# Performance work log

Measured on AMD Instinct MI355X. Metric: run time of the kernel, lower is better.

Reference implementation:

```python
import jax, jax.numpy as jnp
import numpy as np

B, L, D = 16384, 50, 32  # batch, history length, embedding_dim
NU, NI, NC = 100000, 100000, 1000


def setup_inputs() -> dict:
    key = jax.random.key(0)
    ks = jax.random.split(key, 16)
    customer_id = jax.random.randint(ks[0], (B,), 0, NU)
    candidate_good = jax.random.randint(ks[1], (B,), 0, NI)
    candidate_class = jax.random.randint(ks[2], (B,), 0, NC)
    history_goods = jax.random.randint(ks[3], (B, L), 0, NI)
    history_classes = jax.random.randint(ks[4], (B, L), 0, NC)
    user_table = jax.random.normal(ks[5], (NU, D), jnp.float32) * 0.05
    item_table = jax.random.normal(ks[6], (NI, D), jnp.float32) * 0.05
    item_table = item_table.at[0].set(0.0)  # padding_idx=0
    cat_table = jax.random.normal(ks[7], (NC, D), jnp.float32) * 0.05
    cat_table = cat_table.at[0].set(0.0)  # padding_idx=0
    # attention net: Linear(4*2D=256 -> 80), Linear(80 -> 1)
    aw1 = jax.random.normal(ks[8], (4 * 2 * D, 80), jnp.float32) * 0.05
    ab1 = jnp.zeros((80,), jnp.float32)
    aw2 = jax.random.normal(ks[9], (80, 1), jnp.float32) * 0.05
    ab2 = jnp.zeros((1,), jnp.float32)
    # final mlp: 5D=160 -> 256 -> 128 -> 1
    mw1 = jax.random.normal(ks[10], (5 * D, 256), jnp.float32) * 0.05
    mb1 = jnp.zeros((256,), jnp.float32)
    mw2 = jax.random.normal(ks[11], (256, 128), jnp.float32) * 0.05
    mb2 = jnp.zeros((128,), jnp.float32)
    mw3 = jax.random.normal(ks[12], (128, 1), jnp.float32) * 0.05
    mb3 = jnp.zeros((1,), jnp.float32)
    return dict(customer_id=customer_id, candidate_good=candidate_good,
                candidate_class=candidate_class, history_goods=history_goods,
                history_classes=history_classes, user_table=user_table,
                item_table=item_table, cat_table=cat_table,
                aw1=aw1, ab1=ab1, aw2=aw2, ab2=ab2,
                mw1=mw1, mb1=mb1, mw2=mw2, mb2=mb2, mw3=mw3, mb3=mb3)


def reference(customer_id, candidate_good, candidate_class, history_goods,
              history_classes, user_table, item_table, cat_table,
              aw1, ab1, aw2, ab2, mw1, mb1, mw2, mb2, mw3, mb3):
    user_emb = user_table[customer_id]                               # [B, D]
    cand = jnp.concatenate([item_table[candidate_good],
                            cat_table[candidate_class]], axis=-1)    # [B, 2D]
    hist = jnp.concatenate([item_table[history_goods],
                            cat_table[history_classes]], axis=-1)    # [B, L, 2D]
    q = jnp.broadcast_to(cand[:, None, :], hist.shape)               # [B, L, 2D]
    info = jnp.concatenate([q, hist, q - hist, q * hist], axis=-1)   # [B, L, 8D]
    h = jax.nn.relu(info @ aw1 + ab1)                                # [B, L, 80]
    scores = (h @ aw2 + ab2)[..., 0]                                 # [B, L]
    mask = history_goods != 0
    scores = jnp.where(mask, scores, -1e9)
    weights = jax.nn.softmax(scores, axis=1)                         # [B, L]
    att = jnp.einsum('bl,bld->bd', weights, hist)                    # [B, 2D]
    combined = jnp.concatenate([user_emb, cand, att], axis=-1)       # [B, 5D]
    z = jax.nn.relu(combined @ mw1 + mb1)
    z = jax.nn.relu(z @ mw2 + mb2)
    out = (z @ mw3 + mb3)[..., 0]                                    # [B]
    return out
```

## Files before the change

kernel.cpp:

```cpp
#include <hip/hip_runtime.h>
#include <math.h>

#define LHIST 50

typedef __attribute__((ext_vector_type(8))) short bf16x8;
typedef __attribute__((ext_vector_type(4))) float f32x4;

__device__ __forceinline__ unsigned short f2bf(float f) {
    union { float f; unsigned u; } v; v.f = f;
    unsigned r = v.u + 0x7fff + ((v.u >> 16) & 1);
    return (unsigned short)(r >> 16);
}
__device__ __forceinline__ float bf2f(unsigned short h) {
    union { unsigned u; float f; } v; v.u = ((unsigned)h) << 16;
    return v.f;
}


__global__ void prep_kernel(const float* __restrict__ aw1,
                            const float* __restrict__ mw1,
                            const float* __restrict__ mw2,
                            const float* __restrict__ item_table,
                            const float* __restrict__ cat_table,
                            int itemN, int catN,
                            float* __restrict__ Awt,
                            unsigned short* __restrict__ Bmfb,
                            unsigned short* __restrict__ W4fb,
                            unsigned short* __restrict__ W1f,
                            unsigned short* __restrict__ W2f,
                            unsigned short* __restrict__ itemb,
                            unsigned short* __restrict__ catb) {
    int i = blockIdx.x * 256 + threadIdx.x;
    int i8 = i * 8;
    if (i8 + 7 < itemN) {
        float4 a = *(const float4*)&item_table[i8];
        float4 b = *(const float4*)&item_table[i8 + 4];
        ushort4 lo, hi;
        lo.x = f2bf(a.x); lo.y = f2bf(a.y); lo.z = f2bf(a.z); lo.w = f2bf(a.w);
        hi.x = f2bf(b.x); hi.y = f2bf(b.y); hi.z = f2bf(b.z); hi.w = f2bf(b.w);
        *(ushort4*)&itemb[i8] = lo;
        *(ushort4*)&itemb[i8 + 4] = hi;
    }
    if (i8 + 7 < catN) {
        float4 a = *(const float4*)&cat_table[i8];
        float4 b = *(const float4*)&cat_table[i8 + 4];
        ushort4 lo, hi;
        lo.x = f2bf(a.x); lo.y = f2bf(a.y); lo.z = f2bf(a.z); lo.w = f2bf(a.w);
        hi.x = f2bf(b.x); hi.y = f2bf(b.y); hi.z = f2bf(b.z); hi.w = f2bf(b.w);
        *(ushort4*)&catb[i8] = lo;
        *(ushort4*)&catb[i8 + 4] = hi;
    }
    if (i < 5120) {
        int j = i >> 6, k = i & 63;
        Awt[i] = aw1[k * 80 + j] + aw1[(128 + k) * 80 + j];
        int kk = i / 80, n = i - kk * 80;
        int nt = n >> 4, colw = n & 15, ks = kk >> 5, r = kk & 31, qd = r >> 3, off = r & 7;
        int d = ((nt * 2 + ks) * 64 + qd * 16 + colw) * 8 + off;
        Bmfb[d] = f2bf(aw1[(64 + kk) * 80 + n] - aw1[(128 + kk) * 80 + n]);
        W4fb[d] = f2bf(aw1[(192 + kk) * 80 + n]);
    }
    if (i < 40960) {
        int kk = i >> 8, n = i & 255;
        int nt = n >> 4, colw = n & 15, ks = kk >> 5, r = kk & 31, qd = r >> 3, off = r & 7;
        W1f[((nt * 5 + ks) * 64 + qd * 16 + colw) * 8 + off] = f2bf(mw1[i]);
    }
    if (i < 32768) {
        int kk = i >> 7, n = i & 127;
        int nt = n >> 4, colw = n & 15, ks = kk >> 5, r = kk & 31, qd = r >> 3, off = r & 7;
        W2f[((nt * 8 + ks) * 64 + qd * 16 + colw) * 8 + off] = f2bf(mw2[i]);
    }
}

__global__ void __launch_bounds__(256, 6) attn_kernel(
    const int* __restrict__ cid, const int* __restrict__ cg,
    const int* __restrict__ cc,  const int* __restrict__ hg,
    const int* __restrict__ hc,
    const float* __restrict__ user_table, const float* __restrict__ item_table,
    const float* __restrict__ cat_table,
    const float* __restrict__ ab1, const float* __restrict__ aw2,
    const float* __restrict__ Awt, const unsigned short* __restrict__ Bmfb,
    const unsigned short* __restrict__ W4fb,
    const unsigned short* __restrict__ itemb, const unsigned short* __restrict__ catb,
    float* __restrict__ combined)
{
    __shared__ __align__(16) unsigned short sh_Bq[2][5120];
    __shared__ __align__(16) float sh_q[2][64];
    __shared__ float sh_bias[2][80];
    __shared__ float sh_sc[2][64];
    __shared__ float sh_aw2[80];
    __shared__ __align__(16) float sh_att[2][2][64];

    const int t = threadIdx.x;
    const int b0 = blockIdx.x * 2;
    const int wv = t >> 6;
    const int lane = t & 63;
    const int quad = lane >> 4;
    const int col = lane & 15;

    if (t < 128) {
        int qbi = t >> 6, k = t & 63;
        int b = b0 + qbi;
        float v = (k < 32) ? item_table[(size_t)cg[b] * 32 + k]
                           : cat_table[(size_t)cc[b] * 32 + (k - 32)];
        sh_q[qbi][k] = v;
    }
    if (t < 80) sh_aw2[t] = aw2[t];
    __syncthreads();

    for (int i8 = t; i8 < 1280; i8 += 256) {
        int b = i8 >= 640;
        int base = (i8 - b * 640) * 8;
        int lane8 = (base >> 3) & 63, ks = (base >> 9) & 1;
        int kk = ks * 32 + (lane8 >> 4) * 8;
        uint4 bm4 = *(const uint4*)&Bmfb[base];
        uint4 w44 = *(const uint4*)&W4fb[base];
        float4 qa = *(const float4*)&sh_q[b][kk];
        float4 qb = *(const float4*)&sh_q[b][kk + 4];
        unsigned bmw[4] = {bm4.x, bm4.y, bm4.z, bm4.w};
        unsigned w4w[4] = {w44.x, w44.y, w44.z, w44.w};
        float qv[8] = {qa.x, qa.y, qa.z, qa.w, qb.x, qb.y, qb.z, qb.w};
        unsigned res[4];
        #pragma unroll
        for (int d = 0; d < 4; ++d) {
            float b_lo = bf2f((unsigned short)(bmw[d] & 0xffff));
            float b_hi = bf2f((unsigned short)(bmw[d] >> 16));
            float w_lo = bf2f((unsigned short)(w4w[d] & 0xffff));
            float w_hi = bf2f((unsigned short)(w4w[d] >> 16));
            unsigned short r_lo = f2bf(b_lo + qv[2 * d] * w_lo);
            unsigned short r_hi = f2bf(b_hi + qv[2 * d + 1] * w_hi);
            res[d] = (unsigned)r_lo | ((unsigned)r_hi << 16);
        }
        *(uint4*)&sh_Bq[b][base] = make_uint4(res[0], res[1], res[2], res[3]);
    }
    if (t < 160) {
        int bi = t >= 80;
        int j = t - bi * 80;
        float s = ab1[j];
        const float4* aw = (const float4*)&Awt[j * 64];
        #pragma unroll
        for (int k4 = 0; k4 < 16; ++k4) {
            float4 a = aw[k4];
            float4 q = *(const float4*)&sh_q[bi][k4 * 4];
            s += a.x * q.x + a.y * q.y + a.z * q.z + a.w * q.w;
        }
        sh_bias[bi][j] = s;
    }

    const int bb = wv >> 1;
    const int hwv = wv & 1;
    const int b = b0 + bb;
    bf16x8 afr[2][2];
    #pragma unroll
    for (int mi = 0; mi < 2; ++mi) {
        int l = hwv * 32 + mi * 16 + col;
        bool valid = (l < LHIST);
        int lc = valid ? l : 0;
        int idx_i = hg[b * LHIST + lc];
        int idx_c = hc[b * LHIST + lc];
        uint4 vi = *(const uint4*)&itemb[(size_t)idx_i * 32 + quad * 8];
        uint4 vc = *(const uint4*)&catb[(size_t)idx_c * 32 + quad * 8];
        if (!valid) { vi = make_uint4(0, 0, 0, 0); vc = make_uint4(0, 0, 0, 0); }
        afr[mi][0] = *(bf16x8*)&vi;
        afr[mi][1] = *(bf16x8*)&vc;
    }
    __syncthreads();

    f32x4 acc[2][5];
    #pragma unroll
    for (int mi = 0; mi < 2; ++mi)
        #pragma unroll
        for (int nt = 0; nt < 5; ++nt)
            acc[mi][nt] = (f32x4){0.f, 0.f, 0.f, 0.f};

    #pragma unroll
    for (int ks = 0; ks < 2; ++ks) {
        #pragma unroll
        for (int nt = 0; nt < 5; ++nt) {
            bf16x8 bfr = *(const bf16x8*)&sh_Bq[bb][((nt * 2 + ks) * 64 + lane) * 8];
            acc[0][nt] = __builtin_amdgcn_mfma_f32_16x16x32_bf16(afr[0][ks], bfr, acc[0][nt], 0, 0, 0);
            acc[1][nt] = __builtin_amdgcn_mfma_f32_16x16x32_bf16(afr[1][ks], bfr, acc[1][nt], 0, 0, 0);
        }
    }

    {
        float bias_v[5], a2_v[5];
        #pragma unroll
        for (int nt = 0; nt < 5; ++nt) {
            bias_v[nt] = sh_bias[bb][nt * 16 + col];
            a2_v[nt]   = sh_aw2[nt * 16 + col];
        }
        #pragma unroll
        for (int mi = 0; mi < 2; ++mi) {
            int lbase = hwv * 32 + mi * 16 + quad * 4;
            #pragma unroll
            for (int i = 0; i < 4; ++i) {
                float p = 0.f;
                #pragma unroll
                for (int nt = 0; nt < 5; ++nt) {
                    float u = acc[mi][nt][i] + bias_v[nt];
                    p += fmaxf(u, 0.f) * a2_v[nt];
                }
                p += __shfl_xor(p, 1);
                p += __shfl_xor(p, 2);
                p += __shfl_xor(p, 4);
                p += __shfl_xor(p, 8);
                if (col == 0 && lbase + i < 64) sh_sc[bb][lbase + i] = p;
            }
        }
    }
    __syncthreads();

    {
        float sc = -INFINITY;
        if (lane < LHIST) {
            sc = sh_sc[bb][lane];
            if (hg[b * LHIST + lane] == 0) sc = -1e9f;
        }
        float m = sc;
        #pragma unroll
        for (int off = 32; off > 0; off >>= 1) m = fmaxf(m, __shfl_xor(m, off));
        float e = (lane < LHIST) ? __expf(sc - m) : 0.f;
        float ssum = e;
        #pragma unroll
        for (int off = 32; off > 0; off >>= 1) ssum += __shfl_xor(ssum, off);
        float w = e / ssum;

        int c = lane & 7, lgrp = lane >> 3;
        int isCat = c >> 2, s4 = c & 3;
        float at[8];
        #pragma unroll
        for (int j = 0; j < 8; ++j) at[j] = 0.f;
        #pragma unroll
        for (int it = 0; it < 4; ++it) {
            int l = hwv * 32 + it * 8 + lgrp;
            int lc = (l < LHIST) ? l : LHIST - 1;
            float wl = __shfl(w, l);
            int idx = (isCat ? hc : hg)[b * LHIST + lc];
            uint4 hv = *(const uint4*)&(isCat ? catb : itemb)[(size_t)idx * 32 + s4 * 8];
            bf16x8 h = *(bf16x8*)&hv;
            #pragma unroll
            for (int j = 0; j < 8; ++j)
                at[j] += wl * bf2f((unsigned short)h[j]);
        }
        #pragma unroll
        for (int off = 8; off < 64; off <<= 1)
            #pragma unroll
            for (int j = 0; j < 8; ++j) at[j] += __shfl_xor(at[j], off);
        if (lane < 8) {
            *(float4*)&sh_att[bb][hwv][lane * 8]     = make_float4(at[0], at[1], at[2], at[3]);
            *(float4*)&sh_att[bb][hwv][lane * 8 + 4] = make_float4(at[4], at[5], at[6], at[7]);
        }
    }
    __syncthreads();

    if (wv < 2) {
        int bo = b0 + wv;
        float att = sh_att[wv][0][lane] + sh_att[wv][1][lane];
        float* crow = combined + (size_t)bo * 160;
        crow[32 + lane] = sh_q[wv][lane];
        crow[96 + lane] = att;
        if (lane < 32) crow[lane] = user_table[(size_t)cid[bo] * 32 + lane];
    }
}

__global__ void __launch_bounds__(256, 4) mlp_kernel(
    const float* __restrict__ combined,
    const unsigned short* __restrict__ W1f, const unsigned short* __restrict__ W2f,
    const float* __restrict__ mb1, const float* __restrict__ mb2,
    const float* __restrict__ mw3, const float* __restrict__ mb3,
    float* __restrict__ out)
{
    __shared__ __align__(16) unsigned short shA1[5120];
    __shared__ __align__(16) unsigned short shA2[8192];
    __shared__ float sh_part[4][32];

    const int t = threadIdx.x;
    const int b0 = blockIdx.x * 32;
    const int wv = t >> 6;
    const int lane = t & 63;
    const int quad = lane >> 4;
    const int col = lane & 15;

    for (int i = t; i < 1280; i += 256) {
        int m = i / 40;
        int s = i - m * 40;
        int k0 = s * 4;
        float4 v = *(const float4*)&combined[(size_t)(b0 + m) * 160 + k0];
        int mt = m >> 4, colm = m & 15;
        int ks = k0 >> 5, qd = (k0 >> 3) & 3, off = k0 & 7;
        ushort4 r; r.x = f2bf(v.x); r.y = f2bf(v.y); r.z = f2bf(v.z); r.w = f2bf(v.w);
        *(ushort4*)&shA1[((mt * 5 + ks) * 64 + qd * 16 + colm) * 8 + off] = r;
    }
    __syncthreads();

    f32x4 acc1[2][4];
    #pragma unroll
    for (int mt = 0; mt < 2; ++mt)
        #pragma unroll
        for (int j = 0; j < 4; ++j) acc1[mt][j] = (f32x4){0.f, 0.f, 0.f, 0.f};
    #pragma unroll
    for (int ks = 0; ks < 5; ++ks) {
        bf16x8 a0 = *(const bf16x8*)&shA1[(ks * 64 + lane) * 8];
        bf16x8 a1 = *(const bf16x8*)&shA1[((5 + ks) * 64 + lane) * 8];
        #pragma unroll
        for (int j = 0; j < 4; ++j) {
            int ntg = wv * 4 + j;
            bf16x8 b = *(const bf16x8*)&W1f[((ntg * 5 + ks) * 64 + lane) * 8];
            acc1[0][j] = __builtin_amdgcn_mfma_f32_16x16x32_bf16(a0, b, acc1[0][j], 0, 0, 0);
            acc1[1][j] = __builtin_amdgcn_mfma_f32_16x16x32_bf16(a1, b, acc1[1][j], 0, 0, 0);
        }
    }
    #pragma unroll
    for (int j = 0; j < 4; ++j) {
        int n = (wv * 4 + j) * 16 + col;
        float bj = mb1[n];
        int ks2 = n >> 5, qd2 = (n >> 3) & 3, off2 = n & 7;
        #pragma unroll
        for (int mt = 0; mt < 2; ++mt)
            #pragma unroll
            for (int i = 0; i < 4; ++i) {
                float z = fmaxf(acc1[mt][j][i] + bj, 0.f);
                shA2[((mt * 8 + ks2) * 64 + qd2 * 16 + quad * 4 + i) * 8 + off2] = f2bf(z);
            }
    }
    __syncthreads();

    f32x4 acc2[2][2];
    #pragma unroll
    for (int mt = 0; mt < 2; ++mt)
        #pragma unroll
        for (int jj = 0; jj < 2; ++jj) acc2[mt][jj] = (f32x4){0.f, 0.f, 0.f, 0.f};
    #pragma unroll
    for (int ks = 0; ks < 8; ++ks) {
        bf16x8 a0 = *(const bf16x8*)&shA2[(ks * 64 + lane) * 8];
        bf16x8 a1 = *(const bf16x8*)&shA2[((8 + ks) * 64 + lane) * 8];
        #pragma unroll
        for (int jj = 0; jj < 2; ++jj) {
            int ntg = wv * 2 + jj;
            bf16x8 b = *(const bf16x8*)&W2f[((ntg * 8 + ks) * 64 + lane) * 8];
            acc2[0][jj] = __builtin_amdgcn_mfma_f32_16x16x32_bf16(a0, b, acc2[0][jj], 0, 0, 0);
            acc2[1][jj] = __builtin_amdgcn_mfma_f32_16x16x32_bf16(a1, b, acc2[1][jj], 0, 0, 0);
        }
    }
    #pragma unroll
    for (int mt = 0; mt < 2; ++mt) {
        #pragma unroll
        for (int i = 0; i < 4; ++i) {
            float p = 0.f;
            #pragma unroll
            for (int jj = 0; jj < 2; ++jj) {
                int n = (wv * 2 + jj) * 16 + col;
                float z = fmaxf(acc2[mt][jj][i] + mb2[n], 0.f);
                p += z * mw3[n];
            }
            p += __shfl_xor(p, 1);
            p += __shfl_xor(p, 2);
            p += __shfl_xor(p, 4);
            p += __shfl_xor(p, 8);
            if (col == 0) sh_part[wv][mt * 16 + quad * 4 + i] = p;
        }
    }
    __syncthreads();
    if (t < 32)
        out[b0 + t] = sh_part[0][t] + sh_part[1][t] + sh_part[2][t] + sh_part[3][t] + mb3[0];
}

extern "C" void kernel_launch(void* const* d_in, const int* in_sizes, int n_in,
                              void* d_out, int out_size, void* d_ws, size_t ws_size,
                              hipStream_t stream) {
    const int*   cid = (const int*)d_in[0];
    const int*   cg  = (const int*)d_in[1];
    const int*   cc  = (const int*)d_in[2];
    const int*   hg  = (const int*)d_in[3];
    const int*   hc  = (const int*)d_in[4];
    const float* user_table = (const float*)d_in[5];
    const float* item_table = (const float*)d_in[6];
    const float* cat_table  = (const float*)d_in[7];
    const float* aw1 = (const float*)d_in[8];
    const float* ab1 = (const float*)d_in[9];
    const float* aw2 = (const float*)d_in[10];
    const float* mw1 = (const float*)d_in[12];
    const float* mb1 = (const float*)d_in[13];
    const float* mw2 = (const float*)d_in[14];
    const float* mb2 = (const float*)d_in[15];
    const float* mw3 = (const float*)d_in[16];
    const float* mb3 = (const float*)d_in[17];
    float* out = (float*)d_out;

    const int B = in_sizes[0];
    const int itemN = in_sizes[6];
    const int catN  = in_sizes[7];
    float* ws = (float*)d_ws;
    float* Awt = ws;
    unsigned short* Bmfb = (unsigned short*)(ws + 5120);
    unsigned short* W4fb = (unsigned short*)(ws + 7680);
    unsigned short* W1f  = (unsigned short*)(ws + 10240);
    unsigned short* W2f  = (unsigned short*)(ws + 30720);
    unsigned short* itemb = (unsigned short*)(ws + 47104);
    unsigned short* catb  = itemb + itemN;
    float* combined = ws + 47104 + (itemN + catN + 1) / 2;

    int n8 = (itemN + 7) / 8;
    int prep_grid = (n8 + 255) / 256;
    if (prep_grid < 160) prep_grid = 160;
    prep_kernel<<<prep_grid, 256, 0, stream>>>(aw1, mw1, mw2, item_table, cat_table,
                                               itemN, catN, Awt, Bmfb, W4fb, W1f, W2f,
                                               itemb, catb);
    attn_kernel<<<B / 2, 256, 0, stream>>>(cid, cg, cc, hg, hc,
                                           user_table, item_table, cat_table,
                                           ab1, aw2, Awt, Bmfb, W4fb, itemb, catb, combined);
    mlp_kernel<<<B / 32, 256, 0, stream>>>(combined, W1f, W2f,
                                           mb1, mb2, mw3, mb3, out);
}
```

Measured before the change: 198.7 us.

## Share attention weights across batch rows; compute q*hist on A side; emit bf16 MFMA fragments

The attention kernel now handles four batch rows per block with one wave per row. Instead of folding the candidate into a per-row B matrix, it loads the shared Bm and W4 weight fragments once into LDS and forms the q*hist product on the A operand, so K doubles to 128. Each wave walks the whole history, which removes the cross-wave att reduction and several block syncs. The combined vector is written straight into a bf16 MFMA-fragment layout that the MLP kernel reads directly, with 16 rows per block instead of 32. This trades more MFMA work and per-element conversions for less LDS prep and fewer syncs, and it lowers launch bounds occupancy from 6 to 4.

```diff
diff --git a/kernel.cpp b/kernel.cpp
--- a/kernel.cpp
+++ b/kernel.cpp
@@ -71,7 +71,15 @@
     }
 }
 
-__global__ void __launch_bounds__(256, 6) attn_kernel(
+__device__ __forceinline__ bf16x8 hq_frag(uint4 v, const float* qp) {
+    union { uint4 u; unsigned short s[8]; } in; in.u = v;
+    bf16x8 r;
+    #pragma unroll
+    for (int j = 0; j < 8; ++j) r[j] = (short)f2bf(bf2f(in.s[j]) * qp[j]);
+    return r;
+}
+
+__global__ void __launch_bounds__(256, 4) attn_kernel(
     const int* __restrict__ cid, const int* __restrict__ cg,
     const int* __restrict__ cc,  const int* __restrict__ hg,
     const int* __restrict__ hc,
@@ -81,233 +89,240 @@
     const float* __restrict__ Awt, const unsigned short* __restrict__ Bmfb,
     const unsigned short* __restrict__ W4fb,
     const unsigned short* __restrict__ itemb, const unsigned short* __restrict__ catb,
-    float* __restrict__ combined)
+    unsigned short* __restrict__ cfrag)
 {
-    __shared__ __align__(16) unsigned short sh_Bq[2][5120];
-    __shared__ __align__(16) float sh_q[2][64];
-    __shared__ float sh_bias[2][80];
-    __shared__ float sh_sc[2][64];
+    __shared__ __align__(16) unsigned short sh_B[20 * 64 * 8];
+    __shared__ __align__(16) float sh_q[4][64];
+    __shared__ float sh_bias[4][80];
+    __shared__ float sh_sc[4][64];
     __shared__ float sh_aw2[80];
-    __shared__ __align__(16) float sh_att[2][2][64];
 
     const int t = threadIdx.x;
-    const int b0 = blockIdx.x * 2;
+    const int b0 = blockIdx.x * 4;
     const int wv = t >> 6;
     const int lane = t & 63;
     const int quad = lane >> 4;
     const int col = lane & 15;
 
-    if (t < 128) {
-        int qbi = t >> 6, k = t & 63;
+    for (int i = t; i < 1280; i += 256) {
+        int lane8 = i & 63;
+        int ksnt = i >> 6;
+        int nt = ksnt >> 2, ks = ksnt & 3;
+        const unsigned short* src = (ks < 2)
+            ? &Bmfb[((nt * 2 + ks) * 64 + lane8) * 8]
+            : &W4fb[((nt * 2 + (ks - 2)) * 64 + lane8) * 8];
+        *(uint4*)&sh_B[i * 8] = *(const uint4*)src;
+    }
+    {
+        int qbi = wv;
         int b = b0 + qbi;
-        float v = (k < 32) ? item_table[(size_t)cg[b] * 32 + k]
-                           : cat_table[(size_t)cc[b] * 32 + (k - 32)];
-        sh_q[qbi][k] = v;
+        float v = (lane < 32) ? item_table[(size_t)cg[b] * 32 + lane]
+                              : cat_table[(size_t)cc[b] * 32 + (lane - 32)];
+        sh_q[qbi][lane] = v;
     }
     if (t < 80) sh_aw2[t] = aw2[t];
     __syncthreads();
 
-    for (int i8 = t; i8 < 1280; i8 += 256) {
-        int b = i8 >= 640;
-        int base = (i8 - b * 640) * 8;
-        int lane8 = (base >> 3) & 63, ks = (base >> 9) & 1;
-        int kk = ks * 32 + (lane8 >> 4) * 8;
-        uint4 bm4 = *(const uint4*)&Bmfb[base];
-        uint4 w44 = *(const uint4*)&W4fb[base];
-        float4 qa = *(const float4*)&sh_q[b][kk];
-        float4 qb = *(const float4*)&sh_q[b][kk + 4];
-        unsigned bmw[4] = {bm4.x, bm4.y, bm4.z, bm4.w};
-        unsigned w4w[4] = {w44.x, w44.y, w44.z, w44.w};
-        float qv[8] = {qa.x, qa.y, qa.z, qa.w, qb.x, qb.y, qb.z, qb.w};
-        unsigned res[4];
-        #pragma unroll
-        for (int d = 0; d < 4; ++d) {
-            float b_lo = bf2f((unsigned short)(bmw[d] & 0xffff));
-            float b_hi = bf2f((unsigned short)(bmw[d] >> 16));
-            float w_lo = bf2f((unsigned short)(w4w[d] & 0xffff));
-            float w_hi = bf2f((unsigned short)(w4w[d] >> 16));
-            unsigned short r_lo = f2bf(b_lo + qv[2 * d] * w_lo);
-            unsigned short r_hi = f2bf(b_hi + qv[2 * d + 1] * w_hi);
-            res[d] = (unsigned)r_lo | ((unsigned)r_hi << 16);
-        }
-        *(uint4*)&sh_Bq[b][base] = make_uint4(res[0], res[1], res[2], res[3]);
-    }
-    if (t < 160) {
-        int bi = t >= 80;
-        int j = t - bi * 80;
-        float s = ab1[j];
+    const int b = b0 + wv;
+
+    int il[4], ic[4];
+    #pragma unroll
+    for (int mt = 0; mt < 4; ++mt) {
+        int l = mt * 16 + col;
+        int lc = (l < LHIST) ? l : 0;
+        il[mt] = hg[b * LHIST + lc];
+        ic[mt] = hc[b * LHIST + lc];
+    }
+    uint4 vi0 = *(const uint4*)&itemb[(size_t)il[0] * 32 + quad * 8];
+    uint4 vc0 = *(const uint4*)&catb[(size_t)ic[0] * 32 + quad * 8];
+    uint4 vi1 = *(const uint4*)&itemb[(size_t)il[1] * 32 + quad * 8];
+    uint4 vc1 = *(const uint4*)&catb[(size_t)ic[1] * 32 + quad * 8];
+
+    for (int s = t; s < 320; s += 256) {
+        int bi = s / 80, j = s - bi * 80;
+        float acc = ab1[j];
         const float4* aw = (const float4*)&Awt[j * 64];
         #pragma unroll
         for (int k4 = 0; k4 < 16; ++k4) {
             float4 a = aw[k4];
             float4 q = *(const float4*)&sh_q[bi][k4 * 4];
-            s += a.x * q.x + a.y * q.y + a.z * q.z + a.w * q.w;
-        }
-        sh_bias[bi][j] = s;
-    }
-
-    const int bb = wv >> 1;
-    const int hwv = wv & 1;
-    const int b = b0 + bb;
-    bf16x8 afr[2][2];
-    #pragma unroll
-    for (int mi = 0; mi < 2; ++mi) {
-        int l = hwv * 32 + mi * 16 + col;
-        bool valid = (l < LHIST);
-        int lc = valid ? l : 0;
-        int idx_i = hg[b * LHIST + lc];
-        int idx_c = hc[b * LHIST + lc];
-        uint4 vi = *(const uint4*)&itemb[(size_t)idx_i * 32 + quad * 8];
-        uint4 vc = *(const uint4*)&catb[(size_t)idx_c * 32 + quad * 8];
-        if (!valid) { vi = make_uint4(0, 0, 0, 0); vc = make_uint4(0, 0, 0, 0); }
-        afr[mi][0] = *(bf16x8*)&vi;
-        afr[mi][1] = *(bf16x8*)&vc;
+            acc += a.x * q.x + a.y * q.y + a.z * q.z + a.w * q.w;
+        }
+        sh_bias[bi][j] = acc;
     }
     __syncthreads();
 
-    f32x4 acc[2][5];
-    #pragma unroll
-    for (int mi = 0; mi < 2; ++mi)
-        #pragma unroll
-        for (int nt = 0; nt < 5; ++nt)
-            acc[mi][nt] = (f32x4){0.f, 0.f, 0.f, 0.f};
-
-    #pragma unroll
-    for (int ks = 0; ks < 2; ++ks) {
-        #pragma unroll
-        for (int nt = 0; nt < 5; ++nt) {
-            bf16x8 bfr = *(const bf16x8*)&sh_Bq[bb][((nt * 2 + ks) * 64 + lane) * 8];
-            acc[0][nt] = __builtin_amdgcn_mfma_f32_16x16x32_bf16(afr[0][ks], bfr, acc[0][nt], 0, 0, 0);
-            acc[1][nt] = __builtin_amdgcn_mfma_f32_16x16x32_bf16(afr[1][ks], bfr, acc[1][nt], 0, 0, 0);
-        }
-    }
-
+    float q0[8], q1[8];
     {
-        float bias_v[5], a2_v[5];
-        #pragma unroll
-        for (int nt = 0; nt < 5; ++nt) {
-            bias_v[nt] = sh_bias[bb][nt * 16 + col];
-            a2_v[nt]   = sh_aw2[nt * 16 + col];
+        float4 qa = *(const float4*)&sh_q[wv][quad * 8];
+        float4 qb = *(const float4*)&sh_q[wv][quad * 8 + 4];
+        q0[0]=qa.x; q0[1]=qa.y; q0[2]=qa.z; q0[3]=qa.w; q0[4]=qb.x; q0[5]=qb.y; q0[6]=qb.z; q0[7]=qb.w;
+        float4 qc = *(const float4*)&sh_q[wv][32 + quad * 8];
+        float4 qdv = *(const float4*)&sh_q[wv][32 + quad * 8 + 4];
+        q1[0]=qc.x; q1[1]=qc.y; q1[2]=qc.z; q1[3]=qc.w; q1[4]=qdv.x; q1[5]=qdv.y; q1[6]=qdv.z; q1[7]=qdv.w;
+    }
+    float bias_v[5], a2_v[5];
+    #pragma unroll
+    for (int nt = 0; nt < 5; ++nt) {
+        bias_v[nt] = sh_bias[wv][nt * 16 + col];
+        a2_v[nt]   = sh_aw2[nt * 16 + col];
+    }
+
+    #pragma unroll
+    for (int p = 0; p < 2; ++p) {
+        bf16x8 afr[2][4];
+        uint4 vi[2], vc[2];
+        if (p == 0) { vi[0] = vi0; vc[0] = vc0; vi[1] = vi1; vc[1] = vc1; }
+        else {
+            vi[0] = *(const uint4*)&itemb[(size_t)il[2] * 32 + quad * 8];
+            vc[0] = *(const uint4*)&catb[(size_t)ic[2] * 32 + quad * 8];
+            vi[1] = *(const uint4*)&itemb[(size_t)il[3] * 32 + quad * 8];
+            vc[1] = *(const uint4*)&catb[(size_t)ic[3] * 32 + quad * 8];
+            if (48 + col >= LHIST) { vi[1] = make_uint4(0,0,0,0); vc[1] = make_uint4(0,0,0,0); }
         }
         #pragma unroll
         for (int mi = 0; mi < 2; ++mi) {
-            int lbase = hwv * 32 + mi * 16 + quad * 4;
+            afr[mi][0] = *(bf16x8*)&vi[mi];
+            afr[mi][1] = *(bf16x8*)&vc[mi];
+            afr[mi][2] = hq_frag(vi[mi], q0);
+            afr[mi][3] = hq_frag(vc[mi], q1);
+        }
+        f32x4 acc[2][5];
+        #pragma unroll
+        for (int mi = 0; mi < 2; ++mi)
+            #pragma unroll
+            for (int nt = 0; nt < 5; ++nt) acc[mi][nt] = (f32x4){0.f,0.f,0.f,0.f};
+        #pragma unroll
+        for (int ks = 0; ks < 4; ++ks) {
+            #pragma unroll
+            for (int nt = 0; nt < 5; ++nt) {
+                bf16x8 bfr = *(const bf16x8*)&sh_B[((nt * 4 + ks) * 64 + lane) * 8];
+                acc[0][nt] = __builtin_amdgcn_mfma_f32_16x16x32_bf16(afr[0][ks], bfr, acc[0][nt], 0, 0, 0);
+                acc[1][nt] = __builtin_amdgcn_mfma_f32_16x16x32_bf16(afr[1][ks], bfr, acc[1][nt], 0, 0, 0);
+            }
+        }
+        #pragma unroll
+        for (int mi = 0; mi < 2; ++mi) {
+            int mt = p * 2 + mi;
             #pragma unroll
             for (int i = 0; i < 4; ++i) {
-                float p = 0.f;
+                float pp = 0.f;
                 #pragma unroll
                 for (int nt = 0; nt < 5; ++nt) {
                     float u = acc[mi][nt][i] + bias_v[nt];
-                    p += fmaxf(u, 0.f) * a2_v[nt];
+                    pp += fmaxf(u, 0.f) * a2_v[nt];
                 }
-                p += __shfl_xor(p, 1);
-                p += __shfl_xor(p, 2);
-                p += __shfl_xor(p, 4);
-                p += __shfl_xor(p, 8);
-                if (col == 0 && lbase + i < 64) sh_sc[bb][lbase + i] = p;
+                pp += __shfl_xor(pp, 1);
+                pp += __shfl_xor(pp, 2);
+                pp += __shfl_xor(pp, 4);
+                pp += __shfl_xor(pp, 8);
+                if (col == 0) sh_sc[wv][mt * 16 + quad * 4 + i] = pp;
             }
         }
     }
-    __syncthreads();
+
+    float sc = -INFINITY;
+    if (lane < LHIST) {
+        sc = sh_sc[wv][lane];
+        if (hg[b * LHIST + lane] == 0) sc = -1e9f;
+    }
+    float m = sc;
+    #pragma unroll
+    for (int off = 32; off > 0; off >>= 1) m = fmaxf(m, __shfl_xor(m, off));
+    float e = (lane < LHIST) ? __expf(sc - m) : 0.f;
+    float ssum = e;
+    #pragma unroll
+    for (int off = 32; off > 0; off >>= 1) ssum += __shfl_xor(ssum, off);
+    float w = e / ssum;
+
+    int c = lane & 7, lgrp = lane >> 3;
+    int isCat = c >> 2, s4 = c & 3;
+    float at[8];
+    #pragma unroll
+    for (int j = 0; j < 8; ++j) at[j] = 0.f;
+    #pragma unroll
+    for (int it = 0; it < 7; ++it) {
+        int l = it * 8 + lgrp;
+        int lc = (l < LHIST) ? l : 0;
+        float wl = __shfl(w, l);
+        int idx = (isCat ? hc : hg)[b * LHIST + lc];
+        uint4 hv = *(const uint4*)&(isCat ? catb : itemb)[(size_t)idx * 32 + s4 * 8];
+        union { uint4 u; unsigned short s[8]; } hh; hh.u = hv;
+        #pragma unroll
+        for (int j = 0; j < 8; ++j) at[j] += wl * bf2f(hh.s[j]);
+    }
+    #pragma unroll
+    for (int off = 8; off < 64; off <<= 1)
+        #pragma unroll
+        for (int j = 0; j < 8; ++j) at[j] += __shfl_xor(at[j], off);
 
     {
-        float sc = -INFINITY;
-        if (lane < LHIST) {
-            sc = sh_sc[bb][lane];
-            if (hg[b * LHIST + lane] == 0) sc = -1e9f;
-        }
-        float m = sc;
-        #pragma unroll
-        for (int off = 32; off > 0; off >>= 1) m = fmaxf(m, __shfl_xor(m, off));
-        float e = (lane < LHIST) ? __expf(sc - m) : 0.f;
-        float ssum = e;
-        #pragma unroll
-        for (int off = 32; off > 0; off >>= 1) ssum += __shfl_xor(ssum, off);
-        float w = e / ssum;
-
-        int c = lane & 7, lgrp = lane >> 3;
-        int isCat = c >> 2, s4 = c & 3;
-        float at[8];
-        #pragma unroll
-        for (int j = 0; j < 8; ++j) at[j] = 0.f;
-        #pragma unroll
-        for (int it = 0; it < 4; ++it) {
-            int l = hwv * 32 + it * 8 + lgrp;
-            int lc = (l < LHIST) ? l : LHIST - 1;
-            float wl = __shfl(w, l);
-            int idx = (isCat ? hc : hg)[b * LHIST + lc];
-            uint4 hv = *(const uint4*)&(isCat ? catb : itemb)[(size_t)idx * 32 + s4 * 8];
-            bf16x8 h = *(bf16x8*)&hv;
-            #pragma unroll
-            for (int j = 0; j < 8; ++j)
-                at[j] += wl * bf2f((unsigned short)h[j]);
-        }
-        #pragma unroll
-        for (int off = 8; off < 64; off <<= 1)
-            #pragma unroll
-            for (int j = 0; j < 8; ++j) at[j] += __shfl_xor(at[j], off);
+        int g = b >> 4, colm = b & 15;
+        unsigned short* base = cfrag + (size_t)g * 2560;
         if (lane < 8) {
-            *(float4*)&sh_att[bb][hwv][lane * 8]     = make_float4(at[0], at[1], at[2], at[3]);
-            *(float4*)&sh_att[bb][hwv][lane * 8 + 4] = make_float4(at[4], at[5], at[6], at[7]);
-        }
-    }
-    __syncthreads();
-
-    if (wv < 2) {
-        int bo = b0 + wv;
-        float att = sh_att[wv][0][lane] + sh_att[wv][1][lane];
-        float* crow = combined + (size_t)bo * 160;
-        crow[32 + lane] = sh_q[wv][lane];
-        crow[96 + lane] = att;
-        if (lane < 32) crow[lane] = user_table[(size_t)cid[bo] * 32 + lane];
+            int k0 = 96 + lane * 8;
+            int ks = k0 >> 5, qd = (k0 >> 3) & 3;
+            ushort4 lo, hi;
+            lo.x = f2bf(at[0]); lo.y = f2bf(at[1]); lo.z = f2bf(at[2]); lo.w = f2bf(at[3]);
+            hi.x = f2bf(at[4]); hi.y = f2bf(at[5]); hi.z = f2bf(at[6]); hi.w = f2bf(at[7]);
+            unsigned short* p = base + ((ks * 64) + qd * 16 + colm) * 8;
+            *(ushort4*)p = lo;
+            *(ushort4*)(p + 4) = hi;
+        } else if (lane < 16) {
+            int cq = lane - 8;
+            int k0 = 32 + cq * 8;
+            int ks = k0 >> 5, qd = (k0 >> 3) & 3;
+            float4 qa = *(const float4*)&sh_q[wv][cq * 8];
+            float4 qb = *(const float4*)&sh_q[wv][cq * 8 + 4];
+            ushort4 lo, hi;
+            lo.x = f2bf(qa.x); lo.y = f2bf(qa.y); lo.z = f2bf(qa.z); lo.w = f2bf(qa.w);
+            hi.x = f2bf(qb.x); hi.y = f2bf(qb.y); hi.z = f2bf(qb.z); hi.w = f2bf(qb.w);
+            unsigned short* p = base + ((ks * 64) + qd * 16 + colm) * 8;
+            *(ushort4*)p = lo;
+            *(ushort4*)(p + 4) = hi;
+        } else if (lane < 20) {
+            int cu = lane - 16;
+            int uidx = cid[b];
+            float4 ua = *(const float4*)&user_table[(size_t)uidx * 32 + cu * 8];
+            float4 ub = *(const float4*)&user_table[(size_t)uidx * 32 + cu * 8 + 4];
+            ushort4 lo, hi;
+            lo.x = f2bf(ua.x); lo.y = f2bf(ua.y); lo.z = f2bf(ua.z); lo.w = f2bf(ua.w);
+            hi.x = f2bf(ub.x); hi.y = f2bf(ub.y); hi.z = f2bf(ub.z); hi.w = f2bf(ub.w);
+            unsigned short* p = base + (cu * 16 + colm) * 8;
+            *(ushort4*)p = lo;
+            *(ushort4*)(p + 4) = hi;
+        }
     }
 }
 
 __global__ void __launch_bounds__(256, 4) mlp_kernel(
-    const float* __restrict__ combined,
+    const unsigned short* __restrict__ cfrag,
     const unsigned short* __restrict__ W1f, const unsigned short* __restrict__ W2f,
     const float* __restrict__ mb1, const float* __restrict__ mb2,
     const float* __restrict__ mw3, const float* __restrict__ mb3,
     float* __restrict__ out)
 {
-    __shared__ __align__(16) unsigned short shA1[5120];
-    __shared__ __align__(16) unsigned short shA2[8192];
-    __shared__ float sh_part[4][32];
+    __shared__ __align__(16) unsigned short shA2[4096];
+    __shared__ float sh_part[4][16];
 
     const int t = threadIdx.x;
-    const int b0 = blockIdx.x * 32;
+    const int g = blockIdx.x;
     const int wv = t >> 6;
     const int lane = t & 63;
     const int quad = lane >> 4;
     const int col = lane & 15;
-
-    for (int i = t; i < 1280; i += 256) {
-        int m = i / 40;
-        int s = i - m * 40;
-        int k0 = s * 4;
-        float4 v = *(const float4*)&combined[(size_t)(b0 + m) * 160 + k0];
-        int mt = m >> 4, colm = m & 15;
-        int ks = k0 >> 5, qd = (k0 >> 3) & 3, off = k0 & 7;
-        ushort4 r; r.x = f2bf(v.x); r.y = f2bf(v.y); r.z = f2bf(v.z); r.w = f2bf(v.w);
-        *(ushort4*)&shA1[((mt * 5 + ks) * 64 + qd * 16 + colm) * 8 + off] = r;
-    }
-    __syncthreads();
-
-    f32x4 acc1[2][4];
-    #pragma unroll
-    for (int mt = 0; mt < 2; ++mt)
-        #pragma unroll
-        for (int j = 0; j < 4; ++j) acc1[mt][j] = (f32x4){0.f, 0.f, 0.f, 0.f};
+    const unsigned short* abase = cfrag + (size_t)g * 2560;
+
+    f32x4 acc1[4];
+    #pragma unroll
+    for (int j = 0; j < 4; ++j) acc1[j] = (f32x4){0.f, 0.f, 0.f, 0.f};
     #pragma unroll
     for (int ks = 0; ks < 5; ++ks) {
-        bf16x8 a0 = *(const bf16x8*)&shA1[(ks * 64 + lane) * 8];
-        bf16x8 a1 = *(const bf16x8*)&shA1[((5 + ks) * 64 + lane) * 8];
+        bf16x8 a = *(const bf16x8*)&abase[(ks * 64 + lane) * 8];
         #pragma unroll
         for (int j = 0; j < 4; ++j) {
-            int ntg = wv * 4 + j;
-            bf16x8 b = *(const bf16x8*)&W1f[((ntg * 5 + ks) * 64 + lane) * 8];
-            acc1[0][j] = __builtin_amdgcn_mfma_f32_16x16x32_bf16(a0, b, acc1[0][j], 0, 0, 0);
-            acc1[1][j] = __builtin_amdgcn_mfma_f32_16x16x32_bf16(a1, b, acc1[1][j], 0, 0, 0);
+            bf16x8 bw = *(const bf16x8*)&W1f[(((wv * 4 + j) * 5 + ks) * 64 + lane) * 8];
+            acc1[j] = __builtin_amdgcn_mfma_f32_16x16x32_bf16(a, bw, acc1[j], 0, 0, 0);
         }
     }
     #pragma unroll
@@ -316,53 +331,43 @@
         float bj = mb1[n];
         int ks2 = n >> 5, qd2 = (n >> 3) & 3, off2 = n & 7;
         #pragma unroll
-        for (int mt = 0; mt < 2; ++mt)
-            #pragma unroll
-            for (int i = 0; i < 4; ++i) {
-                float z = fmaxf(acc1[mt][j][i] + bj, 0.f);
-                shA2[((mt * 8 + ks2) * 64 + qd2 * 16 + quad * 4 + i) * 8 + off2] = f2bf(z);
-            }
+        for (int i = 0; i < 4; ++i) {
+            float z = fmaxf(acc1[j][i] + bj, 0.f);
+            shA2[(ks2 * 64 + qd2 * 16 + quad * 4 + i) * 8 + off2] = f2bf(z);
+        }
     }
     __syncthreads();
 
-    f32x4 acc2[2][2];
-    #pragma unroll
-    for (int mt = 0; mt < 2; ++mt)
-        #pragma unroll
-        for (int jj = 0; jj < 2; ++jj) acc2[mt][jj] = (f32x4){0.f, 0.f, 0.f, 0.f};
+    f32x4 acc2[2];
+    #pragma unroll
+    for (int jj = 0; jj < 2; ++jj) acc2[jj] = (f32x4){0.f, 0.f, 0.f, 0.f};
     #pragma unroll
     for (int ks = 0; ks < 8; ++ks) {
-        bf16x8 a0 = *(const bf16x8*)&shA2[(ks * 64 + lane) * 8];
-        bf16x8 a1 = *(const bf16x8*)&shA2[((8 + ks) * 64 + lane) * 8];
+        bf16x8 a = *(const bf16x8*)&shA2[(ks * 64 + lane) * 8];
         #pragma unroll
         for (int jj = 0; jj < 2; ++jj) {
-            int ntg = wv * 2 + jj;
-            bf16x8 b = *(const bf16x8*)&W2f[((ntg * 8 + ks) * 64 + lane) * 8];
-            acc2[0][jj] = __builtin_amdgcn_mfma_f32_16x16x32_bf16(a0, b, acc2[0][jj], 0, 0, 0);
-            acc2[1][jj] = __builtin_amdgcn_mfma_f32_16x16x32_bf16(a1, b, acc2[1][jj], 0, 0, 0);
-        }
-    }
-    #pragma unroll
-    for (int mt = 0; mt < 2; ++mt) {
-        #pragma unroll
-        for (int i = 0; i < 4; ++i) {
-            float p = 0.f;
-            #pragma unroll
-            for (int jj = 0; jj < 2; ++jj) {
-                int n = (wv * 2 + jj) * 16 + col;
-                float z = fmaxf(acc2[mt][jj][i] + mb2[n], 0.f);
-                p += z * mw3[n];
-            }
-            p += __shfl_xor(p, 1);
-            p += __shfl_xor(p, 2);
-            p += __shfl_xor(p, 4);
-            p += __shfl_xor(p, 8);
-            if (col == 0) sh_part[wv][mt * 16 + quad * 4 + i] = p;
-        }
+            bf16x8 bw = *(const bf16x8*)&W2f[(((wv * 2 + jj) * 8 + ks) * 64 + lane) * 8];
+            acc2[jj] = __builtin_amdgcn_mfma_f32_16x16x32_bf16(a, bw, acc2[jj], 0, 0, 0);
+        }
+    }
+    #pragma unroll
+    for (int i = 0; i < 4; ++i) {
+        float p = 0.f;
+        #pragma unroll
+        for (int jj = 0; jj < 2; ++jj) {
+            int n = (wv * 2 + jj) * 16 + col;
+            float z = fmaxf(acc2[jj][i] + mb2[n], 0.f);
+            p += z * mw3[n];
+        }
+        p += __shfl_xor(p, 1);
+        p += __shfl_xor(p, 2);
+        p += __shfl_xor(p, 4);
+        p += __shfl_xor(p, 8);
+        if (col == 0) sh_part[wv][quad * 4 + i] = p;
     }
     __syncthreads();
-    if (t < 32)
-        out[b0 + t] = sh_part[0][t] + sh_part[1][t] + sh_part[2][t] + sh_part[3][t] + mb3[0];
+    if (t < 16)
+        out[g * 16 + t] = sh_part[0][t] + sh_part[1][t] + sh_part[2][t] + sh_part[3][t] + mb3[0];
 }
 
 extern "C" void kernel_launch(void* const* d_in, const int* in_sizes, int n_in,
@@ -398,7 +403,7 @@
     unsigned short* W2f  = (unsigned short*)(ws + 30720);
     unsigned short* itemb = (unsigned short*)(ws + 47104);
     unsigned short* catb  = itemb + itemN;
-    float* combined = ws + 47104 + (itemN + catN + 1) / 2;
+    unsigned short* cfrag = (unsigned short*)(ws + 47104 + (itemN + catN + 1) / 2);
 
     int n8 = (itemN + 7) / 8;
     int prep_grid = (n8 + 255) / 256;
@@ -406,9 +411,9 @@
     prep_kernel<<<prep_grid, 256, 0, stream>>>(aw1, mw1, mw2, item_table, cat_table,
                                                itemN, catN, Awt, Bmfb, W4fb, W1f, W2f,
                                                itemb, catb);
-    attn_kernel<<<B / 2, 256, 0, stream>>>(cid, cg, cc, hg, hc,
+    attn_kernel<<<B / 4, 256, 0, stream>>>(cid, cg, cc, hg, hc,
                                            user_table, item_table, cat_table,
-                                           ab1, aw2, Awt, Bmfb, W4fb, itemb, catb, combined);
-    mlp_kernel<<<B / 32, 256, 0, stream>>>(combined, W1f, W2f,
+                                           ab1, aw2, Awt, Bmfb, W4fb, itemb, catb, cfrag);
+    mlp_kernel<<<B / 16, 256, 0, stream>>>(cfrag, W1f, W2f,
                                            mb1, mb2, mw3, mb3, out);
 }
```

Result: no change. 197.6 us (-0.6%).

## Hoist history gathers, swap MFMA operands, reuse gathered rows for attention pooling

Applied to the files above, without the earlier changes.

The attention kernel now issues the history index loads and bf16 embedding gathers at kernel start, before the first barrier, so their latency overlaps the query and weight setup. The MFMA is transposed so weights are the A operand and history rows the B operand, which lets each lane reduce scores with fewer cross-lane shuffles. The weighted pooling reuses the already gathered register rows and reduces them through shared memory instead of gathering the history a second time. Bf16 packing switches to the HIP packed float2-to-bf16 conversion, and the per-batch Bq build shares one weight decode across both batch rows. Invalid history rows past index 49 are no longer zeroed in registers and rely on zero softmax weights instead, and the shared-memory reduction adds LDS traffic.

```diff
diff --git a/kernel.cpp b/kernel.cpp
--- a/kernel.cpp
+++ b/kernel.cpp
@@ -1,4 +1,5 @@
 #include <hip/hip_runtime.h>
+#include <hip/hip_bf16.h>
 #include <math.h>
 
 #define LHIST 50
@@ -15,6 +16,12 @@
     union { unsigned u; float f; } v; v.u = ((unsigned)h) << 16;
     return v.f;
 }
+__device__ __forceinline__ unsigned pk2(float lo, float hi) {
+    __hip_bfloat162 h = __float22bfloat162_rn(make_float2(lo, hi));
+    return *(unsigned*)&h;
+}
+__device__ __forceinline__ float bflo(unsigned u){ union{unsigned v;float f;} x; x.v = u << 16; return x.f; }
+__device__ __forceinline__ float bfhi(unsigned u){ union{unsigned v;float f;} x; x.v = u & 0xffff0000u; return x.f; }
 
 
 __global__ void prep_kernel(const float* __restrict__ aw1,
@@ -35,20 +42,18 @@
     if (i8 + 7 < itemN) {
         float4 a = *(const float4*)&item_table[i8];
         float4 b = *(const float4*)&item_table[i8 + 4];
-        ushort4 lo, hi;
-        lo.x = f2bf(a.x); lo.y = f2bf(a.y); lo.z = f2bf(a.z); lo.w = f2bf(a.w);
-        hi.x = f2bf(b.x); hi.y = f2bf(b.y); hi.z = f2bf(b.z); hi.w = f2bf(b.w);
-        *(ushort4*)&itemb[i8] = lo;
-        *(ushort4*)&itemb[i8 + 4] = hi;
+        uint4 r;
+        r.x = pk2(a.x, a.y); r.y = pk2(a.z, a.w);
+        r.z = pk2(b.x, b.y); r.w = pk2(b.z, b.w);
+        *(uint4*)&itemb[i8] = r;
     }
     if (i8 + 7 < catN) {
         float4 a = *(const float4*)&cat_table[i8];
         float4 b = *(const float4*)&cat_table[i8 + 4];
-        ushort4 lo, hi;
-        lo.x = f2bf(a.x); lo.y = f2bf(a.y); lo.z = f2bf(a.z); lo.w = f2bf(a.w);
-        hi.x = f2bf(b.x); hi.y = f2bf(b.y); hi.z = f2bf(b.z); hi.w = f2bf(b.w);
-        *(ushort4*)&catb[i8] = lo;
-        *(ushort4*)&catb[i8 + 4] = hi;
+        uint4 r;
+        r.x = pk2(a.x, a.y); r.y = pk2(a.z, a.w);
+        r.z = pk2(b.x, b.y); r.w = pk2(b.z, b.w);
+        *(uint4*)&catb[i8] = r;
     }
     if (i < 5120) {
         int j = i >> 6, k = i & 63;
@@ -88,7 +93,7 @@
     __shared__ float sh_bias[2][80];
     __shared__ float sh_sc[2][64];
     __shared__ float sh_aw2[80];
-    __shared__ __align__(16) float sh_att[2][2][64];
+    __shared__ float sh_att[4][64];
 
     const int t = threadIdx.x;
     const int b0 = blockIdx.x * 2;
@@ -96,169 +101,160 @@
     const int lane = t & 63;
     const int quad = lane >> 4;
     const int col = lane & 15;
-
+    const int bb = wv >> 1;
+    const int hwv = wv & 1;
+    const int b = b0 + bb;
+
+    int il[2], ic[2];
+    #pragma unroll
+    for (int mi = 0; mi < 2; ++mi) {
+        int l = hwv * 32 + mi * 16 + col;
+        int lc = (l < LHIST) ? l : 0;
+        il[mi] = hg[b * LHIST + lc];
+        ic[mi] = hc[b * LHIST + lc];
+    }
+    uint4 vi[2], vc[2];
+    #pragma unroll
+    for (int mi = 0; mi < 2; ++mi) {
+        vi[mi] = *(const uint4*)&itemb[(size_t)il[mi] * 32 + quad * 8];
+        vc[mi] = *(const uint4*)&catb[(size_t)ic[mi] * 32 + quad * 8];
+    }
     if (t < 128) {
         int qbi = t >> 6, k = t & 63;
-        int b = b0 + qbi;
-        float v = (k < 32) ? item_table[(size_t)cg[b] * 32 + k]
-                           : cat_table[(size_t)cc[b] * 32 + (k - 32)];
+        int bq = b0 + qbi;
+        float v = (k < 32) ? item_table[(size_t)cg[bq] * 32 + k]
+                           : cat_table[(size_t)cc[bq] * 32 + (k - 32)];
         sh_q[qbi][k] = v;
     }
     if (t < 80) sh_aw2[t] = aw2[t];
     __syncthreads();
 
-    for (int i8 = t; i8 < 1280; i8 += 256) {
-        int b = i8 >= 640;
-        int base = (i8 - b * 640) * 8;
-        int lane8 = (base >> 3) & 63, ks = (base >> 9) & 1;
+    for (int slot = t; slot < 640; slot += 256) {
+        int j = slot * 8;
+        int lane8 = slot & 63, ks = (slot >> 6) & 1;
         int kk = ks * 32 + (lane8 >> 4) * 8;
-        uint4 bm4 = *(const uint4*)&Bmfb[base];
-        uint4 w44 = *(const uint4*)&W4fb[base];
-        float4 qa = *(const float4*)&sh_q[b][kk];
-        float4 qb = *(const float4*)&sh_q[b][kk + 4];
-        unsigned bmw[4] = {bm4.x, bm4.y, bm4.z, bm4.w};
-        unsigned w4w[4] = {w44.x, w44.y, w44.z, w44.w};
-        float qv[8] = {qa.x, qa.y, qa.z, qa.w, qb.x, qb.y, qb.z, qb.w};
-        unsigned res[4];
+        uint4 bm4 = *(const uint4*)&Bmfb[j];
+        uint4 w44 = *(const uint4*)&W4fb[j];
+        unsigned bw[4] = {bm4.x, bm4.y, bm4.z, bm4.w};
+        unsigned ww[4] = {w44.x, w44.y, w44.z, w44.w};
+        float bl[8], wl4[8];
         #pragma unroll
         for (int d = 0; d < 4; ++d) {
-            float b_lo = bf2f((unsigned short)(bmw[d] & 0xffff));
-            float b_hi = bf2f((unsigned short)(bmw[d] >> 16));
-            float w_lo = bf2f((unsigned short)(w4w[d] & 0xffff));
-            float w_hi = bf2f((unsigned short)(w4w[d] >> 16));
-            unsigned short r_lo = f2bf(b_lo + qv[2 * d] * w_lo);
-            unsigned short r_hi = f2bf(b_hi + qv[2 * d + 1] * w_hi);
-            res[d] = (unsigned)r_lo | ((unsigned)r_hi << 16);
-        }
-        *(uint4*)&sh_Bq[b][base] = make_uint4(res[0], res[1], res[2], res[3]);
+            bl[2 * d] = bflo(bw[d]);  bl[2 * d + 1] = bfhi(bw[d]);
+            wl4[2 * d] = bflo(ww[d]); wl4[2 * d + 1] = bfhi(ww[d]);
+        }
+        #pragma unroll
+        for (int bb2 = 0; bb2 < 2; ++bb2) {
+            float4 qa = *(const float4*)&sh_q[bb2][kk];
+            float4 qb = *(const float4*)&sh_q[bb2][kk + 4];
+            float qv[8] = {qa.x, qa.y, qa.z, qa.w, qb.x, qb.y, qb.z, qb.w};
+            uint4 res;
+            unsigned* rp = (unsigned*)&res;
+            #pragma unroll
+            for (int d = 0; d < 4; ++d)
+                rp[d] = pk2(bl[2 * d]     + qv[2 * d]     * wl4[2 * d],
+                            bl[2 * d + 1] + qv[2 * d + 1] * wl4[2 * d + 1]);
+            *(uint4*)&sh_Bq[bb2][j] = res;
+        }
     }
     if (t < 160) {
         int bi = t >= 80;
         int j = t - bi * 80;
-        float s = ab1[j];
+        float acc = ab1[j];
         const float4* aw = (const float4*)&Awt[j * 64];
         #pragma unroll
         for (int k4 = 0; k4 < 16; ++k4) {
             float4 a = aw[k4];
             float4 q = *(const float4*)&sh_q[bi][k4 * 4];
-            s += a.x * q.x + a.y * q.y + a.z * q.z + a.w * q.w;
-        }
-        sh_bias[bi][j] = s;
-    }
-
-    const int bb = wv >> 1;
-    const int hwv = wv & 1;
-    const int b = b0 + bb;
-    bf16x8 afr[2][2];
-    #pragma unroll
-    for (int mi = 0; mi < 2; ++mi) {
-        int l = hwv * 32 + mi * 16 + col;
-        bool valid = (l < LHIST);
-        int lc = valid ? l : 0;
-        int idx_i = hg[b * LHIST + lc];
-        int idx_c = hc[b * LHIST + lc];
-        uint4 vi = *(const uint4*)&itemb[(size_t)idx_i * 32 + quad * 8];
-        uint4 vc = *(const uint4*)&catb[(size_t)idx_c * 32 + quad * 8];
-        if (!valid) { vi = make_uint4(0, 0, 0, 0); vc = make_uint4(0, 0, 0, 0); }
-        afr[mi][0] = *(bf16x8*)&vi;
-        afr[mi][1] = *(bf16x8*)&vc;
-    }
-    __syncthreads();
-
-    f32x4 acc[2][5];
-    #pragma unroll
-    for (int mi = 0; mi < 2; ++mi)
-        #pragma unroll
-        for (int nt = 0; nt < 5; ++nt)
-            acc[mi][nt] = (f32x4){0.f, 0.f, 0.f, 0.f};
-
-    #pragma unroll
-    for (int ks = 0; ks < 2; ++ks) {
-        #pragma unroll
-        for (int nt = 0; nt < 5; ++nt) {
-            bf16x8 bfr = *(const bf16x8*)&sh_Bq[bb][((nt * 2 + ks) * 64 + lane) * 8];
-            acc[0][nt] = __builtin_amdgcn_mfma_f32_16x16x32_bf16(afr[0][ks], bfr, acc[0][nt], 0, 0, 0);
-            acc[1][nt] = __builtin_amdgcn_mfma_f32_16x16x32_bf16(afr[1][ks], bfr, acc[1][nt], 0, 0, 0);
-        }
-    }
+            acc += a.x * q.x + a.y * q.y + a.z * q.z + a.w * q.w;
+        }
+        sh_bias[bi][j] = acc;
+    }
+    __syncthreads();
+
+    float4 a2v[5], bv[5];
+    #pragma unroll
+    for (int jt = 0; jt < 5; ++jt) {
+        a2v[jt] = *(const float4*)&sh_aw2[jt * 16 + quad * 4];
+        bv[jt]  = *(const float4*)&sh_bias[bb][jt * 16 + quad * 4];
+    }
+
+    bf16x8 hi0 = *(bf16x8*)&vi[0];
+    bf16x8 hc0 = *(bf16x8*)&vc[0];
+    bf16x8 hi1 = *(bf16x8*)&vi[1];
+    bf16x8 hc1 = *(bf16x8*)&vc[1];
+    float px = 0.f, py = 0.f;
+    #pragma unroll
+    for (int jt = 0; jt < 5; ++jt) {
+        f32x4 a0 = (f32x4){0.f, 0.f, 0.f, 0.f};
+        f32x4 a1 = (f32x4){0.f, 0.f, 0.f, 0.f};
+        bf16x8 A0 = *(const bf16x8*)&sh_Bq[bb][((jt * 2 + 0) * 64 + lane) * 8];
+        bf16x8 A1 = *(const bf16x8*)&sh_Bq[bb][((jt * 2 + 1) * 64 + lane) * 8];
+        a0 = __builtin_amdgcn_mfma_f32_16x16x32_bf16(A0, hi0, a0, 0, 0, 0);
+        a0 = __builtin_amdgcn_mfma_f32_16x16x32_bf16(A1, hc0, a0, 0, 0, 0);
+        a1 = __builtin_amdgcn_mfma_f32_16x16x32_bf16(A0, hi1, a1, 0, 0, 0);
+        a1 = __builtin_amdgcn_mfma_f32_16x16x32_bf16(A1, hc1, a1, 0, 0, 0);
+        const float* bp = (const float*)&bv[jt];
+        const float* ap = (const float*)&a2v[jt];
+        #pragma unroll
+        for (int i = 0; i < 4; ++i) {
+            px += fmaxf(a0[i] + bp[i], 0.f) * ap[i];
+            py += fmaxf(a1[i] + bp[i], 0.f) * ap[i];
+        }
+    }
+    px += __shfl_xor(px, 16); px += __shfl_xor(px, 32);
+    py += __shfl_xor(py, 16); py += __shfl_xor(py, 32);
+    if (quad == 0) {
+        sh_sc[bb][hwv * 32 + col] = px;
+        sh_sc[bb][hwv * 32 + 16 + col] = py;
+    }
+    __syncthreads();
+
+    float sc = -INFINITY;
+    if (lane < LHIST) {
+        sc = sh_sc[bb][lane];
+        if (hg[b * LHIST + lane] == 0) sc = -1e9f;
+    }
+    float m = sc;
+    #pragma unroll
+    for (int off = 32; off > 0; off >>= 1) m = fmaxf(m, __shfl_xor(m, off));
+    float e = (lane < LHIST) ? __expf(sc - m) : 0.f;
+    float ssum = e;
+    #pragma unroll
+    for (int off = 32; off > 0; off >>= 1) ssum += __shfl_xor(ssum, off);
+    float w = e / ssum;
 
     {
-        float bias_v[5], a2_v[5];
-        #pragma unroll
-        for (int nt = 0; nt < 5; ++nt) {
-            bias_v[nt] = sh_bias[bb][nt * 16 + col];
-            a2_v[nt]   = sh_aw2[nt * 16 + col];
-        }
-        #pragma unroll
-        for (int mi = 0; mi < 2; ++mi) {
-            int lbase = hwv * 32 + mi * 16 + quad * 4;
-            #pragma unroll
-            for (int i = 0; i < 4; ++i) {
-                float p = 0.f;
-                #pragma unroll
-                for (int nt = 0; nt < 5; ++nt) {
-                    float u = acc[mi][nt][i] + bias_v[nt];
-                    p += fmaxf(u, 0.f) * a2_v[nt];
-                }
-                p += __shfl_xor(p, 1);
-                p += __shfl_xor(p, 2);
-                p += __shfl_xor(p, 4);
-                p += __shfl_xor(p, 8);
-                if (col == 0 && lbase + i < 64) sh_sc[bb][lbase + i] = p;
-            }
-        }
-    }
-    __syncthreads();
-
-    {
-        float sc = -INFINITY;
-        if (lane < LHIST) {
-            sc = sh_sc[bb][lane];
-            if (hg[b * LHIST + lane] == 0) sc = -1e9f;
-        }
-        float m = sc;
-        #pragma unroll
-        for (int off = 32; off > 0; off >>= 1) m = fmaxf(m, __shfl_xor(m, off));
-        float e = (lane < LHIST) ? __expf(sc - m) : 0.f;
-        float ssum = e;
-        #pragma unroll
-        for (int off = 32; off > 0; off >>= 1) ssum += __shfl_xor(ssum, off);
-        float w = e / ssum;
-
-        int c = lane & 7, lgrp = lane >> 3;
-        int isCat = c >> 2, s4 = c & 3;
-        float at[8];
-        #pragma unroll
-        for (int j = 0; j < 8; ++j) at[j] = 0.f;
-        #pragma unroll
-        for (int it = 0; it < 4; ++it) {
-            int l = hwv * 32 + it * 8 + lgrp;
-            int lc = (l < LHIST) ? l : LHIST - 1;
-            float wl = __shfl(w, l);
-            int idx = (isCat ? hc : hg)[b * LHIST + lc];
-            uint4 hv = *(const uint4*)&(isCat ? catb : itemb)[(size_t)idx * 32 + s4 * 8];
-            bf16x8 h = *(bf16x8*)&hv;
-            #pragma unroll
-            for (int j = 0; j < 8; ++j)
-                at[j] += wl * bf2f((unsigned short)h[j]);
-        }
-        #pragma unroll
-        for (int off = 8; off < 64; off <<= 1)
-            #pragma unroll
-            for (int j = 0; j < 8; ++j) at[j] += __shfl_xor(at[j], off);
-        if (lane < 8) {
-            *(float4*)&sh_att[bb][hwv][lane * 8]     = make_float4(at[0], at[1], at[2], at[3]);
-            *(float4*)&sh_att[bb][hwv][lane * 8 + 4] = make_float4(at[4], at[5], at[6], at[7]);
-        }
+        float wl0 = __shfl(w, hwv * 32 + col);
+        float wl1 = __shfl(w, hwv * 32 + 16 + col);
+        union { uint4 u; unsigned short s[8]; } i0, i1, c0u, c1u;
+        i0.u = vi[0]; i1.u = vi[1]; c0u.u = vc[0]; c1u.u = vc[1];
+        float ati[8], atc[8];
+        #pragma unroll
+        for (int j = 0; j < 8; ++j) {
+            ati[j] = wl0 * bf2f(i0.s[j]) + wl1 * bf2f(i1.s[j]);
+            atc[j] = wl0 * bf2f(c0u.s[j]) + wl1 * bf2f(c1u.s[j]);
+        }
+        float* red = (float*)sh_Bq;
+        float* myrow = red + wv * 1056 + col * 66;
+        #pragma unroll
+        for (int j2 = 0; j2 < 4; ++j2) {
+            *(float2*)&myrow[quad * 8 + j2 * 2]      = make_float2(ati[2 * j2], ati[2 * j2 + 1]);
+            *(float2*)&myrow[33 + quad * 8 + j2 * 2] = make_float2(atc[2 * j2], atc[2 * j2 + 1]);
+        }
+        int colIdx = (lane < 32) ? lane : 33 + (lane - 32);
+        float s = 0.f;
+        #pragma unroll
+        for (int c = 0; c < 16; ++c) s += red[wv * 1056 + c * 66 + colIdx];
+        sh_att[wv][lane] = s;
     }
     __syncthreads();
 
     if (wv < 2) {
         int bo = b0 + wv;
-        float att = sh_att[wv][0][lane] + sh_att[wv][1][lane];
         float* crow = combined + (size_t)bo * 160;
         crow[32 + lane] = sh_q[wv][lane];
-        crow[96 + lane] = att;
+        crow[96 + lane] = sh_att[2 * wv][lane] + sh_att[2 * wv + 1][lane];
         if (lane < 32) crow[lane] = user_table[(size_t)cid[bo] * 32 + lane];
     }
 }
@@ -305,9 +301,9 @@
         #pragma unroll
         for (int j = 0; j < 4; ++j) {
             int ntg = wv * 4 + j;
-            bf16x8 b = *(const bf16x8*)&W1f[((ntg * 5 + ks) * 64 + lane) * 8];
-            acc1[0][j] = __builtin_amdgcn_mfma_f32_16x16x32_bf16(a0, b, acc1[0][j], 0, 0, 0);
-            acc1[1][j] = __builtin_amdgcn_mfma_f32_16x16x32_bf16(a1, b, acc1[1][j], 0, 0, 0);
+            bf16x8 bw = *(const bf16x8*)&W1f[((ntg * 5 + ks) * 64 + lane) * 8];
+            acc1[0][j] = __builtin_amdgcn_mfma_f32_16x16x32_bf16(a0, bw, acc1[0][j], 0, 0, 0);
+            acc1[1][j] = __builtin_amdgcn_mfma_f32_16x16x32_bf16(a1, bw, acc1[1][j], 0, 0, 0);
         }
     }
     #pragma unroll
@@ -337,9 +333,9 @@
         #pragma unroll
         for (int jj = 0; jj < 2; ++jj) {
             int ntg = wv * 2 + jj;
-            bf16x8 b = *(const bf16x8*)&W2f[((ntg * 8 + ks) * 64 + lane) * 8];
-            acc2[0][jj] = __builtin_amdgcn_mfma_f32_16x16x32_bf16(a0, b, acc2[0][jj], 0, 0, 0);
-            acc2[1][jj] = __builtin_amdgcn_mfma_f32_16x16x32_bf16(a1, b, acc2[1][jj], 0, 0, 0);
+            bf16x8 bw = *(const bf16x8*)&W2f[((ntg * 8 + ks) * 64 + lane) * 8];
+            acc2[0][jj] = __builtin_amdgcn_mfma_f32_16x16x32_bf16(a0, bw, acc2[0][jj], 0, 0, 0);
+            acc2[1][jj] = __builtin_amdgcn_mfma_f32_16x16x32_bf16(a1, bw, acc2[1][jj], 0, 0, 0);
         }
     }
     #pragma unroll
```

After: 189.4 us. 1.05x faster.
